# Kernel optimization log

Hardware: AMD Instinct MI355X
Metric: run time of the kernel (lower is better)

The kernel has to match this reference:

```python
import jax, jax.numpy as jnp
import numpy as np

N = 65536      # total points (single batch, multiple of patch_size)
C = 512        # channels
H = 8          # heads
K = 256        # patch (window) size
SCALE = 0.125  # head_dim ** -0.5


def setup_inputs() -> dict:
    key = jax.random.key(0)
    k1, k2, k3, k4 = jax.random.split(key, 4)
    feat = jax.random.normal(k1, (N, C), dtype=jnp.float32)
    # serialized order = permutation of points; inverse undoes it
    order = jax.random.permutation(k2, N).astype(jnp.int64)
    inverse = jnp.argsort(order).astype(jnp.int64)
    Wqkv = jax.random.normal(k3, (C, 3 * C), dtype=jnp.float32) * (C ** -0.5)
    bqkv = jnp.zeros((3 * C,), dtype=jnp.float32)
    Wproj = jax.random.normal(k4, (C, C), dtype=jnp.float32) * (C ** -0.5)
    bproj = jnp.zeros((C,), dtype=jnp.float32)
    return {"feat": feat, "order": order, "inverse": inverse,
            "Wqkv": Wqkv, "bqkv": bqkv, "Wproj": Wproj, "bproj": bproj}


def reference(feat, order, inverse, Wqkv, bqkv, Wproj, bproj):
    d = C // H
    P = N // K  # number of windows
    # QKV projection then gather into serialized patch order
    qkv = feat @ Wqkv + bqkv                    # [N, 3C]
    qkv = qkv[order].reshape(P, K, 3, H, d)     # [P, K, 3, H, d]
    q, k, v = qkv[:, :, 0], qkv[:, :, 1], qkv[:, :, 2]  # each [P, K, H, d]
    # windowed attention within each patch
    scores = jnp.einsum("pkhd,pmhd->phkm", q, k) * SCALE  # [P, H, K, K]
    attn = jax.nn.softmax(scores, axis=-1)
    out = jnp.einsum("phkm,pmhd->pkhd", attn, v)          # [P, K, H, d]
    out = out.reshape(N, C)[inverse]                       # unpad / de-serialize
    return out @ Wproj + bproj
```

## Files before the change

### kernel.cpp

```cpp
#include <hip/hip_runtime.h>
#include <stdint.h>

#define N_TOK 65536
#define CDIM  512
#define C3    1536
#define HEADS 8
#define DHEAD 64
#define KTOK  256
#define PGRP  256

typedef __attribute__((ext_vector_type(8))) short bf16x8;
typedef __attribute__((ext_vector_type(4))) float f32x4;
typedef __attribute__((ext_vector_type(16))) float f32x16;
typedef __attribute__((ext_vector_type(4))) unsigned u32x4;

__device__ __forceinline__ unsigned short f2bf(float f) {
  union { float f; unsigned u; } t; t.f = f;
  return (unsigned short)((t.u + 0x7fffu + ((t.u >> 16) & 1u)) >> 16);
}

__device__ __forceinline__ unsigned cvt_pk_bf16(float lo, float hi) {
  unsigned r;
  asm("v_cvt_pk_bf16_f32 %0, %1, %2" : "=v"(r) : "v"(lo), "v"(hi));
  return r;
}

__global__ __launch_bounds__(256) void cvt_f32_bf16(const float* __restrict__ in,
                                                    unsigned short* __restrict__ out) {
  size_t i = ((size_t)blockIdx.x * 256 + threadIdx.x) * 4;
  float4 v = *(const float4*)(in + i);
  ushort4 o;
  o.x = f2bf(v.x); o.y = f2bf(v.y); o.z = f2bf(v.z); o.w = f2bf(v.w);
  *(ushort4*)(out + i) = o;
}

__global__ __launch_bounds__(256) void transpose_cvt(const float* __restrict__ in,
                                                     unsigned short* __restrict__ out,
                                                     int R, int Cc) {
  __shared__ float tile[32][33];
  int c0 = blockIdx.x * 32, r0 = blockIdx.y * 32;
  int tx = threadIdx.x & 31, ty = threadIdx.x >> 5;
  for (int i = ty; i < 32; i += 8)
    tile[i][tx] = in[(size_t)(r0 + i) * Cc + c0 + tx];
  __syncthreads();
  for (int i = ty; i < 32; i += 8)
    out[(size_t)(c0 + i) * R + r0 + tx] = f2bf(tile[tx][i]);
}

template <int OF32>
__global__ __launch_bounds__(512, 2) void gemm256(const unsigned short* __restrict__ A,
                                                  const unsigned short* __restrict__ Bt,
                                                  const float* __restrict__ bias,
                                                  void* __restrict__ Cout,
                                                  const int* __restrict__ gather,
                                                  int Nn, int Kk, int nbn) {
  __shared__ __align__(16) unsigned short As[2][256 * 64];
  __shared__ __align__(16) unsigned short Bs[2][256 * 64];

  int cpx = gridDim.x >> 3;
  int wk = (blockIdx.x & 7) * cpx + (blockIdx.x >> 3);
  int bm = wk / nbn, bn = wk % nbn;
  int m0 = bm * 256, n0 = bn * 256;

  int tid = threadIdx.x;
  int wv = tid >> 6, ln = tid & 63, g = ln >> 4, c = ln & 15;
  int wr = wv >> 2, wc = wv & 3;
  int NT = Kk >> 6;

  const char* Ab = (const char*)A;
  const char* Bb = (const char*)Bt;
  int lr = tid >> 3;
  int cg = (tid & 7) ^ (lr & 7);
  unsigned aoff[2][2], boff[2][2];
#pragma unroll
  for (int h2 = 0; h2 < 2; ++h2)
#pragma unroll
    for (int j = 0; j < 2; ++j) {
      int row = h2 * 128 + j * 64 + lr;
      int ga = gather ? gather[m0 + row] : (m0 + row);
      aoff[h2][j] = (unsigned)(((size_t)ga * Kk + cg * 8) * 2);
      boff[h2][j] = (unsigned)(((size_t)(n0 + row) * Kk + cg * 8) * 2);
    }

#define STAGE_A(t, h2) do { int _s = (t) & 1; unsigned _k = (unsigned)(t) * 128u;             \
    __builtin_amdgcn_global_load_lds(                                                          \
        (__attribute__((address_space(1))) void*)(void*)(Ab + aoff[h2][0] + _k),               \
        (__attribute__((address_space(3))) void*)&As[_s][((h2) * 1024 + wv * 64) * 8],         \
        16, 0, 0);                                                                             \
    __builtin_amdgcn_global_load_lds(                                                          \
        (__attribute__((address_space(1))) void*)(void*)(Ab + aoff[h2][1] + _k),               \
        (__attribute__((address_space(3))) void*)&As[_s][((h2) * 1024 + 512 + wv * 64) * 8],   \
        16, 0, 0);                                                                             \
  } while (0)
#define STAGE_B(t, h2) do { int _s = (t) & 1; unsigned _k = (unsigned)(t) * 128u;             \
    __builtin_amdgcn_global_load_lds(                                                          \
        (__attribute__((address_space(1))) void*)(void*)(Bb + boff[h2][0] + _k),               \
        (__attribute__((address_space(3))) void*)&Bs[_s][((h2) * 1024 + wv * 64) * 8],         \
        16, 0, 0);                                                                             \
    __builtin_amdgcn_global_load_lds(                                                          \
        (__attribute__((address_space(1))) void*)(void*)(Bb + boff[h2][1] + _k),               \
        (__attribute__((address_space(3))) void*)&Bs[_s][((h2) * 1024 + 512 + wv * 64) * 8],   \
        16, 0, 0);                                                                             \
  } while (0)
#define RD_A(mi, kc) (*(const bf16x8*)&Ac[((((2 * (mi) + wr) * 16 + c) * 8 + (((kc) * 4 + g) ^ (c & 7))) * 8)])
#define RD_B(ni, kc) (*(const bf16x8*)&Bc[((((4 * (ni) + wc) * 16 + c) * 8 + (((kc) * 4 + g) ^ (c & 7))) * 8)])

  f32x4 acc[8][4];
#pragma unroll
  for (int mi = 0; mi < 8; ++mi)
#pragma unroll
    for (int ni = 0; ni < 4; ++ni)
      acc[mi][ni] = (f32x4){0.f, 0.f, 0.f, 0.f};

  STAGE_A(0, 0); STAGE_A(0, 1); STAGE_B(0, 0); STAGE_B(0, 1);
  STAGE_A(1, 0); STAGE_A(1, 1); STAGE_B(1, 0); STAGE_B(1, 1);
  asm volatile("s_waitcnt vmcnt(8)" ::: "memory");
  __builtin_amdgcn_s_barrier();

  bf16x8 af[4][2], bf[2][2];

#pragma unroll 1
  for (int v = 0; v < NT; ++v) {
    unsigned short* Ac = &As[v & 1][0];
    unsigned short* Bc = &Bs[v & 1][0];

#pragma unroll
    for (int i = 0; i < 4; ++i)
#pragma unroll
      for (int kc = 0; kc < 2; ++kc) af[i][kc] = RD_A(i, kc);
#pragma unroll
    for (int j = 0; j < 2; ++j)
#pragma unroll
      for (int kc = 0; kc < 2; ++kc) bf[j][kc] = RD_B(j, kc);
    if (v >= 1 && v + 1 < NT) STAGE_A(v + 1, 1);
    __builtin_amdgcn_s_barrier();
    asm volatile("s_waitcnt lgkmcnt(0)" ::: "memory");
    __builtin_amdgcn_sched_barrier(0);
    __builtin_amdgcn_s_setprio(1);
#pragma unroll
    for (int i = 0; i < 4; ++i)
#pragma unroll
      for (int j = 0; j < 2; ++j) {
        acc[i][j] = __builtin_amdgcn_mfma_f32_16x16x32_bf16(af[i][0], bf[j][0], acc[i][j], 0, 0, 0);
        acc[i][j] = __builtin_amdgcn_mfma_f32_16x16x32_bf16(af[i][1], bf[j][1], acc[i][j], 0, 0, 0);
      }
    __builtin_amdgcn_s_setprio(0);
    __builtin_amdgcn_s_barrier();

#pragma unroll
    for (int j = 0; j < 2; ++j)
#pragma unroll
      for (int kc = 0; kc < 2; ++kc) bf[j][kc] = RD_B(2 + j, kc);
    if (v >= 1 && v + 1 < NT) STAGE_B(v + 1, 0);
    __builtin_amdgcn_s_barrier();
    asm volatile("s_waitcnt lgkmcnt(0)" ::: "memory");
    __builtin_amdgcn_sched_barrier(0);
    __builtin_amdgcn_s_setprio(1);
#pragma unroll
    for (int i = 0; i < 4; ++i)
#pragma unroll
      for (int j = 0; j < 2; ++j) {
        acc[i][2 + j] = __builtin_amdgcn_mfma_f32_16x16x32_bf16(af[i][0], bf[j][0], acc[i][2 + j], 0, 0, 0);
        acc[i][2 + j] = __builtin_amdgcn_mfma_f32_16x16x32_bf16(af[i][1], bf[j][1], acc[i][2 + j], 0, 0, 0);
      }
    __builtin_amdgcn_s_setprio(0);
    __builtin_amdgcn_s_barrier();

#pragma unroll
    for (int i = 0; i < 4; ++i)
#pragma unroll
      for (int kc = 0; kc < 2; ++kc) af[i][kc] = RD_A(4 + i, kc);
    if (v + 2 < NT) STAGE_A(v + 2, 0);
    __builtin_amdgcn_s_barrier();
    asm volatile("s_waitcnt lgkmcnt(0)" ::: "memory");
    __builtin_amdgcn_sched_barrier(0);
    __builtin_amdgcn_s_setprio(1);
#pragma unroll
    for (int i = 0; i < 4; ++i)
#pragma unroll
      for (int j = 0; j < 2; ++j) {
        acc[4 + i][2 + j] = __builtin_amdgcn_mfma_f32_16x16x32_bf16(af[i][0], bf[j][0], acc[4 + i][2 + j], 0, 0, 0);
        acc[4 + i][2 + j] = __builtin_amdgcn_mfma_f32_16x16x32_bf16(af[i][1], bf[j][1], acc[4 + i][2 + j], 0, 0, 0);
      }
    __builtin_amdgcn_s_setprio(0);
    __builtin_amdgcn_s_barrier();

#pragma unroll
    for (int j = 0; j < 2; ++j)
#pragma unroll
      for (int kc = 0; kc < 2; ++kc) bf[j][kc] = RD_B(j, kc);
    if (v + 2 < NT) STAGE_B(v + 2, 1);
    __builtin_amdgcn_s_barrier();
    asm volatile("s_waitcnt lgkmcnt(0)" ::: "memory");
    __builtin_amdgcn_sched_barrier(0);
    __builtin_amdgcn_s_setprio(1);
#pragma unroll
    for (int i = 0; i < 4; ++i)
#pragma unroll
      for (int j = 0; j < 2; ++j) {
        acc[4 + i][j] = __builtin_amdgcn_mfma_f32_16x16x32_bf16(af[i][0], bf[j][0], acc[4 + i][j], 0, 0, 0);
        acc[4 + i][j] = __builtin_amdgcn_mfma_f32_16x16x32_bf16(af[i][1], bf[j][1], acc[4 + i][j], 0, 0, 0);
      }
    __builtin_amdgcn_s_setprio(0);
    if (v + 2 < NT) asm volatile("s_waitcnt vmcnt(4)" ::: "memory");
    else            asm volatile("s_waitcnt vmcnt(0)" ::: "memory");
    __builtin_amdgcn_s_barrier();
  }

#pragma unroll
  for (int ni = 0; ni < 4; ++ni) {
    int col = n0 + (4 * ni + wc) * 16 + c;
    float bv = bias[col];
#pragma unroll
    for (int mi = 0; mi < 8; ++mi) {
      int rowb = m0 + (2 * mi + wr) * 16 + g * 4;
#pragma unroll
      for (int rr = 0; rr < 4; ++rr) {
        float vv = acc[mi][ni][rr] + bv;
        if (OF32) ((float*)Cout)[(size_t)(rowb + rr) * Nn + col] = vv;
        else ((unsigned short*)Cout)[(size_t)(rowb + rr) * Nn + col] = f2bf(vv);
      }
    }
  }
#undef STAGE_A
#undef STAGE_B
#undef RD_A
#undef RD_B
}

__global__ __launch_bounds__(256, 2) void attn_k(const unsigned short* __restrict__ qkv,
                                                 const int* __restrict__ order,
                                                 unsigned short* __restrict__ attnout) {
  __shared__ __align__(16) unsigned short Ks[KTOK * 64];
  __shared__ __align__(16) unsigned short Vt[64 * 256];

  int p = blockIdx.x >> 3, h = blockIdx.x & 7;
  int tid = threadIdx.x;
  int wv = tid >> 6, ln = tid & 63;
  int lq = ln & 31;
  int hl = ln >> 5;

  const unsigned short* base = qkv + (size_t)p * KTOK * C3 + h * DHEAD;

  {
    int mlo = tid >> 3;
    int j = (tid & 7) ^ (mlo & 7);
    const unsigned short* ksrc = base + CDIM + j * 8;
#pragma unroll
    for (int i = 0; i < 8; ++i) {
      int m = i * 32 + mlo;
      __builtin_amdgcn_global_load_lds(
          (const __attribute__((address_space(1))) void*)(ksrc + (size_t)m * C3),
          (__attribute__((address_space(3))) void*)&Ks[((i << 8) + tid) * 8],
          16, 0, 0);
    }
  }
  {
    const unsigned short* vrow = base + 2 * CDIM + (size_t)tid * C3;
    bf16x8 vv[8];
#pragma unroll
    for (int j = 0; j < 8; ++j) vv[j] = *(const bf16x8*)(vrow + j * 8);
#pragma unroll
    for (int j = 0; j < 8; ++j)
#pragma unroll
      for (int e = 0; e < 8; ++e) {
        int d = j * 8 + e;
        Vt[d * 256 + (((tid >> 3) ^ (d & 7)) << 3) + (tid & 7)] = (unsigned short)vv[j][e];
      }
  }

  bf16x8 qfa[2][4];
  {
    const unsigned short* qr = base + (size_t)(wv * 64 + lq) * C3;
#pragma unroll
    for (int dk = 0; dk < 4; ++dk) qfa[0][dk] = *(const bf16x8*)(qr + dk * 16 + hl * 8);
  }
  __syncthreads();

#pragma unroll
  for (int t = 0; t < 2; ++t) {
    int q0 = wv * 64 + t * 32;
    int ordv[16];
#pragma unroll
    for (int r = 0; r < 16; ++r)
      ordv[r] = order[p * KTOK + q0 + (r & 3) + 8 * (r >> 2) + 4 * hl];

    f32x16 sa[8];
    __builtin_amdgcn_s_setprio(1);
#pragma unroll
    for (int mt = 0; mt < 8; ++mt) {
      f32x16 z;
#pragma unroll
      for (int r = 0; r < 16; ++r) z[r] = 0.f;
      int m = mt * 32 + lq;
#pragma unroll
      for (int dk = 0; dk < 4; ++dk) {
        bf16x8 kf = *(const bf16x8*)&Ks[(m * 8 + ((dk * 2 + hl) ^ (m & 7))) * 8];
        z = __builtin_amdgcn_mfma_f32_32x32x16_bf16(kf, qfa[t][dk], z, 0, 0, 0);
      }
      sa[mt] = z;
    }
    __builtin_amdgcn_s_setprio(0);

    if (t == 0) {
      const unsigned short* qr = base + (size_t)(wv * 64 + 32 + lq) * C3;
#pragma unroll
      for (int dk = 0; dk < 4; ++dk) qfa[1][dk] = *(const bf16x8*)(qr + dk * 16 + hl * 8);
    }

    float mx = sa[0][0];
#pragma unroll
    for (int mt = 0; mt < 8; ++mt)
#pragma unroll
      for (int r = 0; r < 16; ++r) mx = fmaxf(mx, sa[mt][r]);
    mx = fmaxf(mx, __shfl_xor(mx, 32, 64));
    float sum = 0.f;
#pragma unroll
    for (int mt = 0; mt < 8; ++mt)
#pragma unroll
      for (int r = 0; r < 16; ++r) {
        float e = __expf((sa[mt][r] - mx) * 0.125f);
        sa[mt][r] = e;
        sum += e;
      }
    sum += __shfl_xor(sum, 32, 64);
    float inv = 1.f / sum;

    f32x16 oa[2];
#pragma unroll
    for (int r = 0; r < 16; ++r) { oa[0][r] = 0.f; oa[1][r] = 0.f; }
#pragma unroll
    for (int kt = 0; kt < 16; ++kt) {
      int mt = kt >> 1, rb = (kt & 1) * 8;
      unsigned L0 = cvt_pk_bf16(sa[mt][rb + 0] * inv, sa[mt][rb + 1] * inv);
      unsigned L1 = cvt_pk_bf16(sa[mt][rb + 2] * inv, sa[mt][rb + 3] * inv);
      unsigned H0 = cvt_pk_bf16(sa[mt][rb + 4] * inv, sa[mt][rb + 5] * inv);
      unsigned H1 = cvt_pk_bf16(sa[mt][rb + 6] * inv, sa[mt][rb + 7] * inv);
      auto s0 = __builtin_amdgcn_permlane32_swap(L0, H0, false, false);
      auto s1 = __builtin_amdgcn_permlane32_swap(L1, H1, false, false);
      u32x4 pw;
      pw[0] = s0[0]; pw[1] = s1[0]; pw[2] = s0[1]; pw[3] = s1[1];
      bf16x8 pf = __builtin_bit_cast(bf16x8, pw);
      __builtin_amdgcn_s_setprio(1);
#pragma unroll
      for (int dt = 0; dt < 2; ++dt) {
        int d = dt * 32 + lq;
        bf16x8 vf = *(const bf16x8*)&Vt[(d * 32 + ((kt * 2 + hl) ^ (d & 7))) * 8];
        oa[dt] = __builtin_amdgcn_mfma_f32_32x32x16_bf16(pf, vf, oa[dt], 0, 0, 0);
      }
      __builtin_amdgcn_s_setprio(0);
    }

    size_t cb = (size_t)h * DHEAD + lq;
#pragma unroll
    for (int r = 0; r < 16; ++r) {
      size_t rb2 = (size_t)ordv[r] * CDIM + cb;
      attnout[rb2] = f2bf(oa[0][r]);
      attnout[rb2 + 32] = f2bf(oa[1][r]);
    }
  }
}

extern "C" void kernel_launch(void* const* d_in, const int* in_sizes, int n_in,
                              void* d_out, int out_size, void* d_ws, size_t ws_size,
                              hipStream_t stream) {
  const float* feat  = (const float*)d_in[0];
  const int*   order = (const int*)d_in[1];
  const float* Wqkv  = (const float*)d_in[3];
  const float* bqkv  = (const float*)d_in[4];
  const float* Wproj = (const float*)d_in[5];
  const float* bproj = (const float*)d_in[6];
  float* out = (float*)d_out;

  char* ws = (char*)d_ws;
  unsigned short* qkv    = (unsigned short*)ws;
  unsigned short* featb  = (unsigned short*)(ws + (size_t)N_TOK * C3 * 2);
  unsigned short* attn   = featb;
  unsigned short* wqkvT  = (unsigned short*)(ws + (size_t)N_TOK * C3 * 2 + (size_t)N_TOK * CDIM * 2);
  unsigned short* wprojT = wqkvT + C3 * CDIM;

  cvt_f32_bf16<<<(N_TOK * CDIM) / (256 * 4), 256, 0, stream>>>(feat, featb);
  transpose_cvt<<<dim3(C3 / 32, CDIM / 32), 256, 0, stream>>>(Wqkv, wqkvT, CDIM, C3);
  transpose_cvt<<<dim3(CDIM / 32, CDIM / 32), 256, 0, stream>>>(Wproj, wprojT, CDIM, CDIM);

  gemm256<0><<<(N_TOK / 256) * (C3 / 256), 512, 0, stream>>>(
      featb, wqkvT, bqkv, qkv, order, C3, CDIM, C3 / 256);

  attn_k<<<PGRP * HEADS, 256, 0, stream>>>(qkv, order, attn);

  gemm256<1><<<(N_TOK / 256) * (CDIM / 256), 512, 0, stream>>>(
      attn, wprojT, bproj, out, nullptr, CDIM, CDIM, CDIM / 256);
}
```

Baseline: 496.7 us.

## Fuse fp32-to-bf16 feature conversion into QKV GEMM A-tile loads

Removes the separate cvt_f32_bf16 kernel. The QKV GEMM now reads fp32 features directly into registers, converts them with v_cvt_pk_bf16 and writes the bf16 A tile to shared memory, cutting one full read-write pass over the activations. The prefetch schedule is rebuilt from two tiles ahead to a simpler one-tile-ahead double buffer with a full vmcnt(0) wait every iteration, which may expose more load latency. The A loads also no longer go through the global_load_lds DMA path for the fp32 case, which raises register pressure.

```diff
diff --git a/kernel.cpp b/kernel.cpp
--- a/kernel.cpp
+++ b/kernel.cpp
@@ -23,15 +23,6 @@
   unsigned r;
   asm("v_cvt_pk_bf16_f32 %0, %1, %2" : "=v"(r) : "v"(lo), "v"(hi));
   return r;
-}
-
-__global__ __launch_bounds__(256) void cvt_f32_bf16(const float* __restrict__ in,
-                                                    unsigned short* __restrict__ out) {
-  size_t i = ((size_t)blockIdx.x * 256 + threadIdx.x) * 4;
-  float4 v = *(const float4*)(in + i);
-  ushort4 o;
-  o.x = f2bf(v.x); o.y = f2bf(v.y); o.z = f2bf(v.z); o.w = f2bf(v.w);
-  *(ushort4*)(out + i) = o;
 }
 
 __global__ __launch_bounds__(256) void transpose_cvt(const float* __restrict__ in,
@@ -47,8 +38,8 @@
     out[(size_t)(c0 + i) * R + r0 + tx] = f2bf(tile[tx][i]);
 }
 
-template <int OF32>
-__global__ __launch_bounds__(512, 2) void gemm256(const unsigned short* __restrict__ A,
+template <int OF32, int AF32>
+__global__ __launch_bounds__(512, 2) void gemm256(const void* __restrict__ Ain,
                                                   const unsigned short* __restrict__ Bt,
                                                   const float* __restrict__ bias,
                                                   void* __restrict__ Cout,
@@ -67,7 +58,7 @@
   int wr = wv >> 2, wc = wv & 3;
   int NT = Kk >> 6;
 
-  const char* Ab = (const char*)A;
+  const char* Ab = (const char*)Ain;
   const char* Bb = (const char*)Bt;
   int lr = tid >> 3;
   int cg = (tid & 7) ^ (lr & 7);
@@ -78,30 +69,15 @@
     for (int j = 0; j < 2; ++j) {
       int row = h2 * 128 + j * 64 + lr;
       int ga = gather ? gather[m0 + row] : (m0 + row);
-      aoff[h2][j] = (unsigned)(((size_t)ga * Kk + cg * 8) * 2);
+      aoff[h2][j] = (unsigned)(((size_t)ga * Kk + cg * 8) * (AF32 ? 4 : 2));
       boff[h2][j] = (unsigned)(((size_t)(n0 + row) * Kk + cg * 8) * 2);
     }
 
-#define STAGE_A(t, h2) do { int _s = (t) & 1; unsigned _k = (unsigned)(t) * 128u;             \
-    __builtin_amdgcn_global_load_lds(                                                          \
-        (__attribute__((address_space(1))) void*)(void*)(Ab + aoff[h2][0] + _k),               \
-        (__attribute__((address_space(3))) void*)&As[_s][((h2) * 1024 + wv * 64) * 8],         \
-        16, 0, 0);                                                                             \
-    __builtin_amdgcn_global_load_lds(                                                          \
-        (__attribute__((address_space(1))) void*)(void*)(Ab + aoff[h2][1] + _k),               \
-        (__attribute__((address_space(3))) void*)&As[_s][((h2) * 1024 + 512 + wv * 64) * 8],   \
-        16, 0, 0);                                                                             \
-  } while (0)
-#define STAGE_B(t, h2) do { int _s = (t) & 1; unsigned _k = (unsigned)(t) * 128u;             \
-    __builtin_amdgcn_global_load_lds(                                                          \
-        (__attribute__((address_space(1))) void*)(void*)(Bb + boff[h2][0] + _k),               \
-        (__attribute__((address_space(3))) void*)&Bs[_s][((h2) * 1024 + wv * 64) * 8],         \
-        16, 0, 0);                                                                             \
-    __builtin_amdgcn_global_load_lds(                                                          \
-        (__attribute__((address_space(1))) void*)(void*)(Bb + boff[h2][1] + _k),               \
-        (__attribute__((address_space(3))) void*)&Bs[_s][((h2) * 1024 + 512 + wv * 64) * 8],   \
-        16, 0, 0);                                                                             \
-  } while (0)
+#define DMA(src, dst)                                                       \
+  __builtin_amdgcn_global_load_lds(                                          \
+      (const __attribute__((address_space(1))) void*)(const void*)(src),     \
+      (__attribute__((address_space(3))) void*)(dst), 16, 0, 0)
+
 #define RD_A(mi, kc) (*(const bf16x8*)&Ac[((((2 * (mi) + wr) * 16 + c) * 8 + (((kc) * 4 + g) ^ (c & 7))) * 8)])
 #define RD_B(ni, kc) (*(const bf16x8*)&Bc[((((4 * (ni) + wc) * 16 + c) * 8 + (((kc) * 4 + g) ^ (c & 7))) * 8)])
 
@@ -112,17 +88,61 @@
     for (int ni = 0; ni < 4; ++ni)
       acc[mi][ni] = (f32x4){0.f, 0.f, 0.f, 0.f};
 
-  STAGE_A(0, 0); STAGE_A(0, 1); STAGE_B(0, 0); STAGE_B(0, 1);
-  STAGE_A(1, 0); STAGE_A(1, 1); STAGE_B(1, 0); STAGE_B(1, 1);
-  asm volatile("s_waitcnt vmcnt(8)" ::: "memory");
-  __builtin_amdgcn_s_barrier();
-
-  bf16x8 af[4][2], bf[2][2];
+  {
+    unsigned short* An = &As[0][0];
+    unsigned short* Bn = &Bs[0][0];
+    if (AF32) {
+      float4 aw[2][2][2];
+#pragma unroll
+      for (int h2 = 0; h2 < 2; ++h2)
+#pragma unroll
+        for (int j = 0; j < 2; ++j) {
+          const float4* src = (const float4*)(Ab + aoff[h2][j]);
+          aw[h2][j][0] = src[0];
+          aw[h2][j][1] = src[1];
+        }
+      __builtin_amdgcn_sched_barrier(0);
+#pragma unroll
+      for (int h2 = 0; h2 < 2; ++h2) {
+        DMA(Bb + boff[h2][0], &Bn[(h2 * 1024 + wv * 64) * 8]);
+        DMA(Bb + boff[h2][1], &Bn[(h2 * 1024 + 512 + wv * 64) * 8]);
+      }
+#pragma unroll
+      for (int h2 = 0; h2 < 2; ++h2)
+#pragma unroll
+        for (int j = 0; j < 2; ++j) {
+          u32x4 pw;
+          pw[0] = cvt_pk_bf16(aw[h2][j][0].x, aw[h2][j][0].y);
+          pw[1] = cvt_pk_bf16(aw[h2][j][0].z, aw[h2][j][0].w);
+          pw[2] = cvt_pk_bf16(aw[h2][j][1].x, aw[h2][j][1].y);
+          pw[3] = cvt_pk_bf16(aw[h2][j][1].z, aw[h2][j][1].w);
+          *(bf16x8*)&An[(h2 * 1024 + j * 512 + tid) * 8] = __builtin_bit_cast(bf16x8, pw);
+        }
+    } else {
+#pragma unroll
+      for (int h2 = 0; h2 < 2; ++h2) {
+        DMA(Ab + aoff[h2][0], &An[(h2 * 1024 + wv * 64) * 8]);
+        DMA(Ab + aoff[h2][1], &An[(h2 * 1024 + 512 + wv * 64) * 8]);
+        DMA(Bb + boff[h2][0], &Bn[(h2 * 1024 + wv * 64) * 8]);
+        DMA(Bb + boff[h2][1], &Bn[(h2 * 1024 + 512 + wv * 64) * 8]);
+      }
+    }
+    asm volatile("s_waitcnt vmcnt(0) lgkmcnt(0)" ::: "memory");
+    __builtin_amdgcn_s_barrier();
+  }
+
+  bf16x8 af[4][2], bf[4][2];
 
 #pragma unroll 1
   for (int v = 0; v < NT; ++v) {
     unsigned short* Ac = &As[v & 1][0];
     unsigned short* Bc = &Bs[v & 1][0];
+    unsigned short* An = &As[(v + 1) & 1][0];
+    unsigned short* Bn = &Bs[(v + 1) & 1][0];
+    bool st = (v + 1 < NT);
+    unsigned ka = (unsigned)(v + 1) * (AF32 ? 256u : 128u);
+    unsigned kb = (unsigned)(v + 1) * 128u;
+    float4 aw[2][2][2];
 
 #pragma unroll
     for (int i = 0; i < 4; ++i)
@@ -132,7 +152,25 @@
     for (int j = 0; j < 2; ++j)
 #pragma unroll
       for (int kc = 0; kc < 2; ++kc) bf[j][kc] = RD_B(j, kc);
-    if (v >= 1 && v + 1 < NT) STAGE_A(v + 1, 1);
+    if (st) {
+      if (AF32) {
+#pragma unroll
+        for (int h2 = 0; h2 < 2; ++h2)
+#pragma unroll
+          for (int j = 0; j < 2; ++j) {
+            const float4* src = (const float4*)(Ab + aoff[h2][j] + ka);
+            aw[h2][j][0] = src[0];
+            aw[h2][j][1] = src[1];
+          }
+        __builtin_amdgcn_sched_barrier(0);
+      } else {
+#pragma unroll
+        for (int h2 = 0; h2 < 2; ++h2) {
+          DMA(Ab + aoff[h2][0] + ka, &An[(h2 * 1024 + wv * 64) * 8]);
+          DMA(Ab + aoff[h2][1] + ka, &An[(h2 * 1024 + 512 + wv * 64) * 8]);
+        }
+      }
+    }
     __builtin_amdgcn_s_barrier();
     asm volatile("s_waitcnt lgkmcnt(0)" ::: "memory");
     __builtin_amdgcn_sched_barrier(0);
@@ -150,8 +188,14 @@
 #pragma unroll
     for (int j = 0; j < 2; ++j)
 #pragma unroll
-      for (int kc = 0; kc < 2; ++kc) bf[j][kc] = RD_B(2 + j, kc);
-    if (v >= 1 && v + 1 < NT) STAGE_B(v + 1, 0);
+      for (int kc = 0; kc < 2; ++kc) bf[2 + j][kc] = RD_B(2 + j, kc);
+    if (st) {
+#pragma unroll
+      for (int h2 = 0; h2 < 2; ++h2) {
+        DMA(Bb + boff[h2][0] + kb, &Bn[(h2 * 1024 + wv * 64) * 8]);
+        DMA(Bb + boff[h2][1] + kb, &Bn[(h2 * 1024 + 512 + wv * 64) * 8]);
+      }
+    }
     __builtin_amdgcn_s_barrier();
     asm volatile("s_waitcnt lgkmcnt(0)" ::: "memory");
     __builtin_amdgcn_sched_barrier(0);
@@ -160,8 +204,8 @@
     for (int i = 0; i < 4; ++i)
 #pragma unroll
       for (int j = 0; j < 2; ++j) {
-        acc[i][2 + j] = __builtin_amdgcn_mfma_f32_16x16x32_bf16(af[i][0], bf[j][0], acc[i][2 + j], 0, 0, 0);
-        acc[i][2 + j] = __builtin_amdgcn_mfma_f32_16x16x32_bf16(af[i][1], bf[j][1], acc[i][2 + j], 0, 0, 0);
+        acc[i][2 + j] = __builtin_amdgcn_mfma_f32_16x16x32_bf16(af[i][0], bf[2 + j][0], acc[i][2 + j], 0, 0, 0);
+        acc[i][2 + j] = __builtin_amdgcn_mfma_f32_16x16x32_bf16(af[i][1], bf[2 + j][1], acc[i][2 + j], 0, 0, 0);
       }
     __builtin_amdgcn_s_setprio(0);
     __builtin_amdgcn_s_barrier();
@@ -170,7 +214,6 @@
     for (int i = 0; i < 4; ++i)
 #pragma unroll
       for (int kc = 0; kc < 2; ++kc) af[i][kc] = RD_A(4 + i, kc);
-    if (v + 2 < NT) STAGE_A(v + 2, 0);
     __builtin_amdgcn_s_barrier();
     asm volatile("s_waitcnt lgkmcnt(0)" ::: "memory");
     __builtin_amdgcn_sched_barrier(0);
@@ -179,17 +222,25 @@
     for (int i = 0; i < 4; ++i)
 #pragma unroll
       for (int j = 0; j < 2; ++j) {
-        acc[4 + i][2 + j] = __builtin_amdgcn_mfma_f32_16x16x32_bf16(af[i][0], bf[j][0], acc[4 + i][2 + j], 0, 0, 0);
-        acc[4 + i][2 + j] = __builtin_amdgcn_mfma_f32_16x16x32_bf16(af[i][1], bf[j][1], acc[4 + i][2 + j], 0, 0, 0);
+        acc[4 + i][2 + j] = __builtin_amdgcn_mfma_f32_16x16x32_bf16(af[i][0], bf[2 + j][0], acc[4 + i][2 + j], 0, 0, 0);
+        acc[4 + i][2 + j] = __builtin_amdgcn_mfma_f32_16x16x32_bf16(af[i][1], bf[2 + j][1], acc[4 + i][2 + j], 0, 0, 0);
       }
     __builtin_amdgcn_s_setprio(0);
     __builtin_amdgcn_s_barrier();
 
-#pragma unroll
-    for (int j = 0; j < 2; ++j)
-#pragma unroll
-      for (int kc = 0; kc < 2; ++kc) bf[j][kc] = RD_B(j, kc);
-    if (v + 2 < NT) STAGE_B(v + 2, 1);
+    if (st && AF32) {
+#pragma unroll
+      for (int h2 = 0; h2 < 2; ++h2)
+#pragma unroll
+        for (int j = 0; j < 2; ++j) {
+          u32x4 pw;
+          pw[0] = cvt_pk_bf16(aw[h2][j][0].x, aw[h2][j][0].y);
+          pw[1] = cvt_pk_bf16(aw[h2][j][0].z, aw[h2][j][0].w);
+          pw[2] = cvt_pk_bf16(aw[h2][j][1].x, aw[h2][j][1].y);
+          pw[3] = cvt_pk_bf16(aw[h2][j][1].z, aw[h2][j][1].w);
+          *(bf16x8*)&An[(h2 * 1024 + j * 512 + tid) * 8] = __builtin_bit_cast(bf16x8, pw);
+        }
+    }
     __builtin_amdgcn_s_barrier();
     asm volatile("s_waitcnt lgkmcnt(0)" ::: "memory");
     __builtin_amdgcn_sched_barrier(0);
@@ -202,8 +253,7 @@
         acc[4 + i][j] = __builtin_amdgcn_mfma_f32_16x16x32_bf16(af[i][1], bf[j][1], acc[4 + i][j], 0, 0, 0);
       }
     __builtin_amdgcn_s_setprio(0);
-    if (v + 2 < NT) asm volatile("s_waitcnt vmcnt(4)" ::: "memory");
-    else            asm volatile("s_waitcnt vmcnt(0)" ::: "memory");
+    asm volatile("s_waitcnt vmcnt(0) lgkmcnt(0)" ::: "memory");
     __builtin_amdgcn_s_barrier();
   }
 
@@ -222,8 +272,7 @@
       }
     }
   }
-#undef STAGE_A
-#undef STAGE_B
+#undef DMA
 #undef RD_A
 #undef RD_B
 }
@@ -374,20 +423,18 @@
 
   char* ws = (char*)d_ws;
   unsigned short* qkv    = (unsigned short*)ws;
-  unsigned short* featb  = (unsigned short*)(ws + (size_t)N_TOK * C3 * 2);
-  unsigned short* attn   = featb;
+  unsigned short* attn   = (unsigned short*)(ws + (size_t)N_TOK * C3 * 2);
   unsigned short* wqkvT  = (unsigned short*)(ws + (size_t)N_TOK * C3 * 2 + (size_t)N_TOK * CDIM * 2);
   unsigned short* wprojT = wqkvT + C3 * CDIM;
 
-  cvt_f32_bf16<<<(N_TOK * CDIM) / (256 * 4), 256, 0, stream>>>(feat, featb);
   transpose_cvt<<<dim3(C3 / 32, CDIM / 32), 256, 0, stream>>>(Wqkv, wqkvT, CDIM, C3);
   transpose_cvt<<<dim3(CDIM / 32, CDIM / 32), 256, 0, stream>>>(Wproj, wprojT, CDIM, CDIM);
 
-  gemm256<0><<<(N_TOK / 256) * (C3 / 256), 512, 0, stream>>>(
-      featb, wqkvT, bqkv, qkv, order, C3, CDIM, C3 / 256);
+  gemm256<0, 1><<<(N_TOK / 256) * (C3 / 256), 512, 0, stream>>>(
+      feat, wqkvT, bqkv, qkv, order, C3, CDIM, C3 / 256);
 
   attn_k<<<PGRP * HEADS, 256, 0, stream>>>(qkv, order, attn);
 
-  gemm256<1><<<(N_TOK / 256) * (CDIM / 256), 512, 0, stream>>>(
+  gemm256<1, 0><<<(N_TOK / 256) * (CDIM / 256), 512, 0, stream>>>(
       attn, wprojT, bproj, out, nullptr, CDIM, CDIM, CDIM / 256);
 }
```

New measurement: 531.4 us. 1.07x slower.
